# Kernel tuning notes

Hardware: AMD Instinct MI355X
Metric: run time of the kernel (lower is better)

The kernel has to match this reference:

```python
import jax, jax.numpy as jnp
import numpy as np
import math

D = 512          # belief_dim
H = 128          # hidden_dim
R = 64           # relation_dim
M = 8192         # max_beliefs
N = 131072       # candidate pairs
INIT_BIAS = math.log(0.4 / 0.6) * -1.0  # = log(1.5) ~ 0.405465


def _linear_params(key, fan_in, fan_out):
    kw, kb = jax.random.split(key)
    bound = 1.0 / math.sqrt(fan_in)
    W = jax.random.uniform(kw, (fan_in, fan_out), minval=-bound, maxval=bound, dtype=jnp.float32)
    b = jax.random.uniform(kb, (fan_out,), minval=-bound, maxval=bound, dtype=jnp.float32)
    return W, b


def setup_inputs() -> dict:
    key = jax.random.key(0)
    ks = jax.random.split(key, 11)
    beliefs = jax.random.normal(ks[0], (M, D), dtype=jnp.float32)
    src_idx = jax.random.randint(ks[1], (N,), 0, M)
    tgt_idx = jax.random.randint(ks[2], (N,), 0, M)
    # proposal_net: 3D -> H -> H//2 -> 1  (last bias = log(1.5))
    pw1, pb1 = _linear_params(ks[3], 3 * D, H)
    pw2, pb2 = _linear_params(ks[4], H, H // 2)
    pw3, _ = _linear_params(ks[5], H // 2, 1)
    pb3 = jnp.full((1,), INIT_BIAS, dtype=jnp.float32)
    # direction_net: 3D -> H//2 -> 1 (sigmoid)
    dw1, db1 = _linear_params(ks[6], 3 * D, H // 2)
    dw2, db2 = _linear_params(ks[7], H // 2, 1)
    # relation_net: 3D -> H -> R
    rw1, rb1 = _linear_params(ks[8], 3 * D, H)
    rw2, rb2 = _linear_params(ks[9], H, R)
    return {
        "beliefs": beliefs, "src_idx": src_idx, "tgt_idx": tgt_idx,
        "pw1": pw1, "pb1": pb1, "pw2": pw2, "pb2": pb2, "pw3": pw3, "pb3": pb3,
        "dw1": dw1, "db1": db1, "dw2": dw2, "db2": db2,
        "rw1": rw1, "rb1": rb1, "rw2": rw2, "rb2": rb2,
    }


def reference(beliefs, src_idx, tgt_idx,
              pw1, pb1, pw2, pb2, pw3, pb3,
              dw1, db1, dw2, db2,
              rw1, rb1, rw2, rb2):
    src = beliefs[src_idx]                       # [N, D] gather
    tgt = beliefs[tgt_idx]                       # [N, D] gather
    feats = jnp.concatenate([src, tgt, jnp.abs(src - tgt)], axis=-1)  # [N, 3D]

    # proposal head -> edge probability
    h = jax.nn.relu(feats @ pw1 + pb1)
    h = jax.nn.relu(h @ pw2 + pb2)
    probs = jax.nn.sigmoid((h @ pw3 + pb3)[:, 0])                     # [N]

    # direction head -> angle in [0, pi/2]
    d = jax.nn.relu(feats @ dw1 + db1)
    directions = jax.nn.sigmoid((d @ dw2 + db2)[:, 0]) * (jnp.pi / 2)  # [N]

    # relation head -> initial relation vectors
    r = jax.nn.relu(feats @ rw1 + rb1)
    relations = r @ rw2 + rb2                                          # [N, R]

    return probs, directions, relations
```

## Files before the change

kernel.cpp:

```cpp
#include <hip/hip_runtime.h>
#include <hip/hip_bf16.h>


#define DD 512
#define K3 1536
#define ROWS 128
#define RB3 64
#define LDACT 328
#define BUFS 12288
#define BUFS2 16384
#define BUFS3 8192

typedef short bf16x8 __attribute__((ext_vector_type(8)));
typedef float f32x4 __attribute__((ext_vector_type(4)));

__device__ inline float b2f(short s) {
    union { float f; unsigned u; } v;
    v.u = ((unsigned)(unsigned short)s) << 16;
    return v.f;
}
__device__ inline short f2b(float f) {
    union { float fl; unsigned u; } v;
    v.fl = f;
    unsigned x = v.u;
    unsigned r = x + 0x7fffu + ((x >> 16) & 1u);
    return (short)(r >> 16);
}
__device__ inline short babsdiff(short a, short b) {
    union { float f; unsigned u; } v;
    v.f = b2f(a) - b2f(b);
    return (short)((v.u & 0x7fffffffu) >> 16);
}
__device__ __forceinline__ bf16x8 babs8(bf16x8 s, bf16x8 t) {
    bf16x8 a;
#pragma unroll
    for (int j = 0; j < 8; j++) a[j] = babsdiff(s[j], t[j]);
    return a;
}

__device__ __forceinline__ int sidx32(int seg, int rt, int lane) {
    return ((seg * 8 + rt) * 64 + lane) * 8;
}
__device__ __forceinline__ void writeStage(short* buf, int rtw, int lnw, int kcb,
                                           bf16x8 s0, bf16x8 s1,
                                           bf16x8 t0, bf16x8 t1) {
    bf16x8 a0 = babs8(s0, t0), a1 = babs8(s1, t1);
    int l0 = kcb * 16 + lnw, l1 = l0 + 16;
    *(bf16x8*)&buf[sidx32(0, rtw, l0)] = s0;
    *(bf16x8*)&buf[sidx32(0, rtw, l1)] = s1;
    *(bf16x8*)&buf[sidx32(1, rtw, l0)] = t0;
    *(bf16x8*)&buf[sidx32(1, rtw, l1)] = t1;
    *(bf16x8*)&buf[sidx32(2, rtw, l0)] = a0;
    *(bf16x8*)&buf[sidx32(2, rtw, l1)] = a1;
}
__device__ __forceinline__ void stage_f32(const float* bs, const float* bt,
                                          short* buf, int rtw, int lnw, int kcb) {
#pragma unroll
    for (int c = 0; c < 2; c++) {
        bf16x8 sb, tb, ab;
#pragma unroll
        for (int h = 0; h < 2; h++) {
            float4 s4 = ((const float4*)bs)[c * 2 + h];
            float4 t4 = ((const float4*)bt)[c * 2 + h];
            float ss[4] = {s4.x, s4.y, s4.z, s4.w};
            float tt[4] = {t4.x, t4.y, t4.z, t4.w};
#pragma unroll
            for (int e = 0; e < 4; e++) {
                int j = h * 4 + e;
                sb[j] = f2b(ss[e]);
                tb[j] = f2b(tt[e]);
                ab[j] = f2b(fabsf(ss[e] - tt[e]));
            }
        }
        int l16 = (kcb + c) * 16 + lnw;
        *(bf16x8*)&buf[sidx32(0, rtw, l16)] = sb;
        *(bf16x8*)&buf[sidx32(1, rtw, l16)] = tb;
        *(bf16x8*)&buf[sidx32(2, rtw, l16)] = ab;
    }
}

#define WT_ELEMS (320 * 1536)
#define P2T_OFF WT_ELEMS
#define R2T_OFF (WT_ELEMS + 64 * 128)
#define PREP_TOT (WT_ELEMS + 2 * 64 * 128)
#define BEL_ELEMS (8192 * 512)
#define BEL_OFF PREP_TOT

__global__ void prep_kernel(const float* __restrict__ pw1,
                            const float* __restrict__ dw1,
                            const float* __restrict__ rw1,
                            const float* __restrict__ pw2,
                            const float* __restrict__ rw2,
                            const float* __restrict__ beliefs,
                            short* __restrict__ ws, int total8) {
    int i8 = blockIdx.x * 256 + threadIdx.x;
    if (i8 >= total8) return;
    int i = i8 * 8;
    bf16x8 o;
    if (i < WT_ELEMS) {
        int n = i / K3, k = i - n * K3;
        const float* src;
        int stride, off;
        if (n < 128)      { src = pw1; stride = 128; off = n; }
        else if (n < 192) { src = dw1; stride = 64;  off = n - 128; }
        else              { src = rw1; stride = 128; off = n - 192; }
#pragma unroll
        for (int j = 0; j < 8; j++) o[j] = f2b(src[(k + j) * stride + off]);
    } else if (i < R2T_OFF) {
        int jj = i - P2T_OFF;
        int n = jj >> 7, k = jj & 127;
#pragma unroll
        for (int j = 0; j < 8; j++) o[j] = f2b(pw2[(k + j) * 64 + n]);
    } else if (i < PREP_TOT) {
        int jj = i - R2T_OFF;
        int n = jj >> 7, k = jj & 127;
#pragma unroll
        for (int j = 0; j < 8; j++) o[j] = f2b(rw2[(k + j) * 64 + n]);
    } else {
        const float4* b4 = (const float4*)(beliefs + (i - BEL_OFF));
        float4 x = b4[0], y = b4[1];
        float v[8] = {x.x, x.y, x.z, x.w, y.x, y.y, y.z, y.w};
#pragma unroll
        for (int j = 0; j < 8; j++) o[j] = f2b(v[j]);
    }
    *(bf16x8*)&ws[i] = o;
}

__global__ __launch_bounds__(256) void prep_bst(
    const short* __restrict__ bel16, const short* __restrict__ WT,
    float* __restrict__ Bs, float* __restrict__ Bt) {
    const int tb = blockIdx.x & 1;
    const int r0 = (blockIdx.x >> 1) * 32;
    const int t = threadIdx.x;
    const int w = t >> 6, lane = t & 63, q = lane >> 4, ln = lane & 15;
    float* Bo = tb ? Bt : Bs;
    const int koff = tb ? 512 : 0;

    f32x4 acc[5][2];
#pragma unroll
    for (int ct = 0; ct < 5; ct++)
#pragma unroll
        for (int rt = 0; rt < 2; rt++) acc[ct][rt] = (f32x4)(0.f);

#pragma unroll
    for (int k0 = 0; k0 < 512; k0 += 128)
#pragma unroll
        for (int kk = 0; kk < 4; kk++) {
            bf16x8 bfr[5];
#pragma unroll
            for (int ct = 0; ct < 5; ct++)
                bfr[ct] = *(const bf16x8*)(WT + (size_t)(w * 80 + ct * 16 + ln) * K3 +
                                           koff + k0 + kk * 32 + q * 8);
#pragma unroll
            for (int rt = 0; rt < 2; rt++) {
                bf16x8 af = *(const bf16x8*)(bel16 +
                    (size_t)(r0 + rt * 16 + ln) * DD + k0 + kk * 32 + q * 8);
#pragma unroll
                for (int ct = 0; ct < 5; ct++)
                    acc[ct][rt] = __builtin_amdgcn_mfma_f32_16x16x32_bf16(
                        af, bfr[ct], acc[ct][rt], 0, 0, 0);
            }
        }
#pragma unroll
    for (int ct = 0; ct < 5; ct++)
#pragma unroll
        for (int rt = 0; rt < 2; rt++)
#pragma unroll
            for (int i = 0; i < 4; i++)
                Bo[(size_t)(r0 + rt * 16 + q * 4 + i) * 320 +
                   w * 80 + ct * 16 + ln] = acc[ct][rt][i];
}

__global__ __launch_bounds__(256, 3) void edge_main3(
    const short* __restrict__ bel16,
    const int* __restrict__ src_idx, const int* __restrict__ tgt_idx,
    const float* __restrict__ Bs, const float* __restrict__ Bt,
    const float* __restrict__ pb1, const float* __restrict__ db1,
    const float* __restrict__ rb1,
    const float* __restrict__ pb2, const float* __restrict__ pw3,
    const float* __restrict__ pb3,
    const float* __restrict__ dw2, const float* __restrict__ db2,
    const float* __restrict__ rb2,
    const short* __restrict__ WT, const short* __restrict__ pw2T,
    const short* __restrict__ rw2T,
    float* __restrict__ out, int N)
{
    __shared__ __align__(16) char smem_u[32768];
    __shared__ int sIdxR[RB3], tIdxR[RB3];
    short* As = (short*)smem_u;
    short (*acts)[LDACT] = (short (*)[LDACT])smem_u;

    const int t = threadIdx.x;
    const int r0 = blockIdx.x * RB3;
    const int w = t >> 6, lane = t & 63, q = lane >> 4, ln = lane & 15;

    if (t < RB3) sIdxR[t] = src_idx[r0 + t];
    else if (t < 2 * RB3) tIdxR[t - RB3] = tgt_idx[r0 + t - RB3];
    __syncthreads();

    const int rr = t >> 2, cc = t & 3;
    const int rtw = rr >> 4, lnw = rr & 15;
    const size_t srow = (size_t)sIdxR[rr] * DD;
    const size_t trow = (size_t)tIdxR[rr] * DD;

    f32x4 acc[5][4];
#pragma unroll
    for (int ct = 0; ct < 5; ct++)
#pragma unroll
        for (int rt = 0; rt < 4; rt++) acc[ct][rt] = (f32x4)(0.f);

#pragma unroll
    for (int qd = 0; qd < 4; qd++) {
        bf16x8 s8 = *(const bf16x8*)(bel16 + srow + cc * 32 + qd * 8);
        bf16x8 t8 = *(const bf16x8*)(bel16 + trow + cc * 32 + qd * 8);
        bf16x8 a8 = babs8(s8, t8);
        *(bf16x8*)&As[((cc * 4 + rtw) * 64 + qd * 16 + lnw) * 8] = a8;
    }
    __syncthreads();

#pragma unroll
    for (int step = 0; step < 4; step++) {
        short* bufC = As + (step & 1) * BUFS3;
        short* bufN = As + ((step & 1) ^ 1) * BUFS3;
        const int k0 = step * 128;
        const bool pf = (step < 3);
        bf16x8 ps, pt;

#pragma unroll
        for (int kk = 0; kk < 4; kk++) {
            bf16x8 bfr[5];
#pragma unroll
            for (int ct = 0; ct < 5; ct++)
                bfr[ct] = *(const bf16x8*)(WT + (size_t)(w * 80 + ct * 16 + ln) * K3 +
                                           1024 + k0 + kk * 32 + q * 8);
            __builtin_amdgcn_sched_barrier(0);
            if (pf) {
                if (kk > 0) {
                    bf16x8 a8 = babs8(ps, pt);
                    *(bf16x8*)&bufN[((cc * 4 + rtw) * 64 + (kk - 1) * 16 + lnw) * 8] = a8;
                }
                ps = *(const bf16x8*)(bel16 + srow + k0 + 128 + cc * 32 + kk * 8);
                pt = *(const bf16x8*)(bel16 + trow + k0 + 128 + cc * 32 + kk * 8);
            }
            __builtin_amdgcn_sched_barrier(0);
            __builtin_amdgcn_s_setprio(1);
#pragma unroll
            for (int rt = 0; rt < 4; rt++) {
                bf16x8 af = *(const bf16x8*)&bufC[((kk * 4 + rt) * 64 + lane) * 8];
#pragma unroll
                for (int ct = 0; ct < 5; ct++)
                    acc[ct][rt] = __builtin_amdgcn_mfma_f32_16x16x32_bf16(
                        af, bfr[ct], acc[ct][rt], 0, 0, 0);
            }
            __builtin_amdgcn_s_setprio(0);
        }
        if (pf) {
            bf16x8 a8 = babs8(ps, pt);
            *(bf16x8*)&bufN[((cc * 4 + rtw) * 64 + 3 * 16 + lnw) * 8] = a8;
        }
        __syncthreads();
    }

#pragma unroll
    for (int hh = 0; hh < 2; hh++) {
        float bias5[5];
#pragma unroll
        for (int ct = 0; ct < 5; ct++) {
            int col = w * 80 + ct * 16 + ln;
            bias5[ct] = (col < 128) ? pb1[col]
                      : (col < 192) ? db1[col - 128]
                                    : rb1[col - 192];
        }
#pragma unroll
        for (int rt2 = 0; rt2 < 2; rt2++)
#pragma unroll
            for (int i = 0; i < 4; i++) {
                int lrow = rt2 * 16 + q * 4 + i;
                const float* bsp = Bs + (size_t)sIdxR[hh * 32 + lrow] * 320 +
                                   w * 80 + ln;
                const float* btp = Bt + (size_t)tIdxR[hh * 32 + lrow] * 320 +
                                   w * 80 + ln;
#pragma unroll
                for (int ct = 0; ct < 5; ct++) {
                    float v = acc[ct][hh * 2 + rt2][i] +
                              bsp[ct * 16] + btp[ct * 16] + bias5[ct];
                    acts[lrow][w * 80 + ct * 16 + ln] = f2b(fmaxf(v, 0.f));
                }
            }
        __syncthreads();

        {
            f32x4 rc[2];
#pragma unroll
            for (int rt2 = 0; rt2 < 2; rt2++) rc[rt2] = (f32x4)(0.f);
#pragma unroll
            for (int ks = 0; ks < 4; ks++) {
                bf16x8 bfr = *(const bf16x8*)(rw2T + (w * 16 + ln) * 128 +
                                              ks * 32 + q * 8);
#pragma unroll
                for (int rt2 = 0; rt2 < 2; rt2++) {
                    bf16x8 afr = *(const bf16x8*)&acts[rt2 * 16 + ln][192 + ks * 32 + q * 8];
                    rc[rt2] = __builtin_amdgcn_mfma_f32_16x16x32_bf16(afr, bfr, rc[rt2], 0, 0, 0);
                }
            }
            int col = w * 16 + ln;
            float bias = rb2[col];
            float* rel = out + 2 * (size_t)N;
#pragma unroll
            for (int rt2 = 0; rt2 < 2; rt2++)
#pragma unroll
                for (int i = 0; i < 4; i++) {
                    int grow = r0 + hh * 32 + rt2 * 16 + q * 4 + i;
                    rel[(size_t)grow * 64 + col] = rc[rt2][i] + bias;
                }
        }

        f32x4 pc[2];
        {
#pragma unroll
            for (int rt2 = 0; rt2 < 2; rt2++) pc[rt2] = (f32x4)(0.f);
#pragma unroll
            for (int ks = 0; ks < 4; ks++) {
                bf16x8 bfr = *(const bf16x8*)(pw2T + (w * 16 + ln) * 128 +
                                              ks * 32 + q * 8);
#pragma unroll
                for (int rt2 = 0; rt2 < 2; rt2++) {
                    bf16x8 afr = *(const bf16x8*)&acts[rt2 * 16 + ln][0 + ks * 32 + q * 8];
                    pc[rt2] = __builtin_amdgcn_mfma_f32_16x16x32_bf16(afr, bfr, pc[rt2], 0, 0, 0);
                }
            }
        }
        __syncthreads();

        {
            int col = w * 16 + ln;
            float bias = pb2[col];
#pragma unroll
            for (int rt2 = 0; rt2 < 2; rt2++)
#pragma unroll
                for (int i = 0; i < 4; i++) {
                    int lrow = rt2 * 16 + q * 4 + i;
                    acts[lrow][col] = f2b(fmaxf(pc[rt2][i] + bias, 0.f));
                }
        }
        __syncthreads();

        {
            int role = t >> 7;
            int rloc = (t & 127) >> 2;
            int kq = t & 3;
            float s = 0.f;
            if (role == 0) {
#pragma unroll
                for (int j = 0; j < 16; j++)
                    s += b2f(acts[rloc][kq * 16 + j]) * pw3[kq * 16 + j];
            } else {
#pragma unroll
                for (int j = 0; j < 16; j++)
                    s += b2f(acts[rloc][128 + kq * 16 + j]) * dw2[kq * 16 + j];
            }
            s += __shfl_xor(s, 1);
            s += __shfl_xor(s, 2);
            if (kq == 0) {
                if (role == 0) {
                    float pr = 1.f / (1.f + __expf(-(s + pb3[0])));
                    out[r0 + hh * 32 + rloc] = pr;
                } else {
                    float dir = (1.f / (1.f + __expf(-(s + db2[0])))) *
                                1.57079632679489662f;
                    out[(size_t)N + r0 + hh * 32 + rloc] = dir;
                }
            }
        }
        __syncthreads();
    }
}

template<bool BF>
__global__ __launch_bounds__(256, 2) void edge_main(
    const float* __restrict__ beliefs, const short* __restrict__ bel16,
    const int* __restrict__ src_idx, const int* __restrict__ tgt_idx,
    const float* __restrict__ pb1, const float* __restrict__ db1,
    const float* __restrict__ rb1,
    const float* __restrict__ pb2, const float* __restrict__ pw3,
    const float* __restrict__ pb3,
    const float* __restrict__ dw2, const float* __restrict__ db2,
    const float* __restrict__ rb2,
    const short* __restrict__ WT, const short* __restrict__ pw2T,
    const short* __restrict__ rw2T,
    float* __restrict__ out, int N)
{
    __shared__ __align__(16) char smem_u[49152];
    short* As2 = (short*)smem_u;
    short (*acts)[LDACT] = (short (*)[LDACT])smem_u;
    int* sIdx = (int*)smem_u;
    int* tIdx = sIdx + ROWS;

    const int t = threadIdx.x;
    const int r0 = blockIdx.x * ROWS;
    const int w = t >> 6, lane = t & 63, q = lane >> 4, ln = lane & 15;

    if (t < ROWS) sIdx[t] = src_idx[r0 + t] * DD;
    else tIdx[t - ROWS] = tgt_idx[r0 + t - ROWS] * DD;
    __syncthreads();

    const int rrow = t >> 1, kh = t & 1;
    const int rtw = rrow >> 4, lnw = rrow & 15;
    const int kcb = kh * 2;
    const int srow = sIdx[rrow], trow = tIdx[rrow];
    __syncthreads();

    f32x4 acc[5][8];
#pragma unroll
    for (int ct = 0; ct < 5; ct++)
#pragma unroll
        for (int rt = 0; rt < 8; rt++) acc[ct][rt] = (f32x4)(0.f);

    bf16x8 bfr0[5];
#pragma unroll
    for (int ct = 0; ct < 5; ct++) {
        int col = w * 80 + ct * 16 + ln;
        bfr0[ct] = *(const bf16x8*)(WT + (size_t)col * K3 + q * 8);
    }
    if constexpr (BF) {
        const bf16x8* pS = (const bf16x8*)(bel16 + srow + kh * 16);
        const bf16x8* pT = (const bf16x8*)(bel16 + trow + kh * 16);
        writeStage(As2, rtw, lnw, kcb, pS[0], pS[1], pT[0], pT[1]);
    } else {
        stage_f32(beliefs + srow + kh * 16, beliefs + trow + kh * 16,
                  As2, rtw, lnw, kcb);
    }
    __syncthreads();

    for (int step = 0; step < 16; ++step) {
        short* bufC = As2 + (step & 1) * BUFS;
        short* bufN = As2 + ((step & 1) ^ 1) * BUFS;
        const int k0 = step * 32;
        const bool pf = (step < 15);
        bf16x8 ns0, ns1, nt0, nt1;

#pragma unroll
        for (int seg = 0; seg < 3; seg++) {
            bf16x8 bfr[5];
            if (seg == 0) {
#pragma unroll
                for (int ct = 0; ct < 5; ct++) bfr[ct] = bfr0[ct];
            } else {
#pragma unroll
                for (int ct = 0; ct < 5; ct++) {
                    int col = w * 80 + ct * 16 + ln;
                    bfr[ct] = *(const bf16x8*)(WT + (size_t)col * K3 +
                                               seg * DD + k0 + q * 8);
                }
            }
            if (seg == 2) {
                __builtin_amdgcn_sched_barrier(0);
                if (pf) {
                    if constexpr (BF) {
                        const bf16x8* pS = (const bf16x8*)(bel16 + srow + k0 + 32 + kh * 16);
                        const bf16x8* pT = (const bf16x8*)(bel16 + trow + k0 + 32 + kh * 16);
                        ns0 = pS[0]; ns1 = pS[1]; nt0 = pT[0]; nt1 = pT[1];
                    }
#pragma unroll
                    for (int ct = 0; ct < 5; ct++) {
                        int col = w * 80 + ct * 16 + ln;
                        bfr0[ct] = *(const bf16x8*)(WT + (size_t)col * K3 +
                                                    k0 + 32 + q * 8);
                    }
                }
                __builtin_amdgcn_sched_barrier(0);
            }
            __builtin_amdgcn_s_setprio(1);
#pragma unroll
            for (int rt = 0; rt < 8; rt++) {
                bf16x8 af = *(const bf16x8*)&bufC[sidx32(seg, rt, lane)];
#pragma unroll
                for (int ct = 0; ct < 5; ct++)
                    acc[ct][rt] = __builtin_amdgcn_mfma_f32_16x16x32_bf16(
                        af, bfr[ct], acc[ct][rt], 0, 0, 0);
            }
            __builtin_amdgcn_s_setprio(0);
        }
        if constexpr (BF) {
            if (pf) writeStage(bufN, rtw, lnw, kcb, ns0, ns1, nt0, nt1);
        } else {
            if (pf) stage_f32(beliefs + srow + k0 + 32 + kh * 16,
                              beliefs + trow + k0 + 32 + kh * 16,
                              bufN, rtw, lnw, kcb);
        }
        __syncthreads();
    }

#pragma unroll
    for (int h = 0; h < 2; h++) {
#pragma unroll
        for (int ct = 0; ct < 5; ct++) {
            int col = w * 80 + ct * 16 + ln;
            float bias = (col < 128) ? pb1[col]
                       : (col < 192) ? db1[col - 128]
                                     : rb1[col - 192];
#pragma unroll
            for (int rt4 = 0; rt4 < 4; rt4++)
#pragma unroll
                for (int i = 0; i < 4; i++) {
                    int lrow = rt4 * 16 + q * 4 + i;
                    float v = acc[ct][h * 4 + rt4][i] + bias;
                    acts[lrow][col] = f2b(fmaxf(v, 0.f));
                }
        }
        __syncthreads();
        {
            f32x4 rc[4];
#pragma unroll
            for (int rt = 0; rt < 4; rt++) rc[rt] = (f32x4)(0.f);
#pragma unroll
            for (int ks = 0; ks < 4; ks++) {
                bf16x8 bfr = *(const bf16x8*)(rw2T + (w * 16 + ln) * 128 +
                                              ks * 32 + q * 8);
#pragma unroll
                for (int rt = 0; rt < 4; rt++) {
                    bf16x8 afr = *(const bf16x8*)&acts[rt * 16 + ln][192 + ks * 32 + q * 8];
                    rc[rt] = __builtin_amdgcn_mfma_f32_16x16x32_bf16(afr, bfr, rc[rt], 0, 0, 0);
                }
            }
            int col = w * 16 + ln;
            float bias = rb2[col];
            float* rel = out + 2 * (size_t)N;
#pragma unroll
            for (int rt = 0; rt < 4; rt++)
#pragma unroll
                for (int i = 0; i < 4; i++) {
                    int grow = r0 + h * 64 + rt * 16 + q * 4 + i;
                    rel[(size_t)grow * 64 + col] = rc[rt][i] + bias;
                }
        }
        f32x4 pc[4];
        {
#pragma unroll
            for (int rt = 0; rt < 4; rt++) pc[rt] = (f32x4)(0.f);
#pragma unroll
            for (int ks = 0; ks < 4; ks++) {
                bf16x8 bfr = *(const bf16x8*)(pw2T + (w * 16 + ln) * 128 +
                                              ks * 32 + q * 8);
#pragma unroll
                for (int rt = 0; rt < 4; rt++) {
                    bf16x8 afr = *(const bf16x8*)&acts[rt * 16 + ln][0 + ks * 32 + q * 8];
                    pc[rt] = __builtin_amdgcn_mfma_f32_16x16x32_bf16(afr, bfr, pc[rt], 0, 0, 0);
                }
            }
        }
        __syncthreads();
        {
            int col = w * 16 + ln;
            float bias = pb2[col];
#pragma unroll
            for (int rt = 0; rt < 4; rt++)
#pragma unroll
                for (int i = 0; i < 4; i++) {
                    int lrow = rt * 16 + q * 4 + i;
                    acts[lrow][col] = f2b(fmaxf(pc[rt][i] + bias, 0.f));
                }
        }
        __syncthreads();
        if (t < 64) {
            float s = pb3[0];
#pragma unroll 8
            for (int k = 0; k < 64; k++) s += b2f(acts[t][k]) * pw3[k];
            float pr = 1.f / (1.f + __expf(-s));
            out[r0 + h * 64 + t] = pr;
        } else if (t < 128) {
            int lrow = t - 64;
            float s = db2[0];
#pragma unroll 8
            for (int k = 0; k < 64; k++) s += b2f(acts[lrow][128 + k]) * dw2[k];
            float dir = (1.f / (1.f + __expf(-s))) * 1.57079632679489662f;
            out[(size_t)N + r0 + h * 64 + lrow] = dir;
        }
        __syncthreads();
    }
}

extern "C" void kernel_launch(void* const* d_in, const int* in_sizes, int n_in,
                              void* d_out, int out_size, void* d_ws, size_t ws_size,
                              hipStream_t stream) {
    const float* beliefs = (const float*)d_in[0];
    const int* src = (const int*)d_in[1];
    const int* tgt = (const int*)d_in[2];
    const float* pw1 = (const float*)d_in[3];
    const float* pb1 = (const float*)d_in[4];
    const float* pw2 = (const float*)d_in[5];
    const float* pb2 = (const float*)d_in[6];
    const float* pw3 = (const float*)d_in[7];
    const float* pb3 = (const float*)d_in[8];
    const float* dw1 = (const float*)d_in[9];
    const float* db1 = (const float*)d_in[10];
    const float* dw2 = (const float*)d_in[11];
    const float* db2 = (const float*)d_in[12];
    const float* rw1 = (const float*)d_in[13];
    const float* rb1 = (const float*)d_in[14];
    const float* rw2 = (const float*)d_in[15];
    const float* rb2 = (const float*)d_in[16];

    short* ws = (short*)d_ws;
    short* WT    = ws;
    short* pw2T  = ws + P2T_OFF;
    short* rw2T  = ws + R2T_OFF;
    short* bel16 = ws + BEL_OFF;
    const int N = in_sizes[1];

    const size_t BF_BYTES = (size_t)(PREP_TOT + BEL_ELEMS) * sizeof(short);
    const size_t FULL_BYTES = BF_BYTES + (size_t)2 * 8192 * 320 * sizeof(float);
    const bool useV2 = ws_size >= FULL_BYTES;
    const bool useBf = ws_size >= BF_BYTES;
    const int prepElems = useBf ? (PREP_TOT + BEL_ELEMS) : PREP_TOT;
    const int prep8 = prepElems / 8;

    prep_kernel<<<(prep8 + 255) / 256, 256, 0, stream>>>(
        pw1, dw1, rw1, pw2, rw2, beliefs, ws, prep8);

    if (useV2) {
        float* Bsp = (float*)(ws + PREP_TOT + BEL_ELEMS);
        float* Btp = Bsp + (size_t)8192 * 320;
        prep_bst<<<512, 256, 0, stream>>>(bel16, WT, Bsp, Btp);
        edge_main3<<<N / RB3, 256, 0, stream>>>(
            bel16, src, tgt, Bsp, Btp,
            pb1, db1, rb1, pb2, pw3, pb3, dw2, db2, rb2,
            WT, pw2T, rw2T, (float*)d_out, N);
    } else if (useBf) {
        edge_main<true><<<N / ROWS, 256, 0, stream>>>(
            beliefs, bel16, src, tgt, pb1, db1, rb1, pb2, pw3, pb3,
            dw2, db2, rb2, WT, pw2T, rw2T, (float*)d_out, N);
    } else {
        edge_main<false><<<N / ROWS, 256, 0, stream>>>(
            beliefs, bel16, src, tgt, pb1, db1, rb1, pb2, pw3, pb3,
            dw2, db2, rb2, WT, pw2T, rw2T, (float*)d_out, N);
    }
}
```

Before: 271.3 us.

## Split edge kernel into per-wave 32-row tiles with bf16 precomputed src/tgt tables

The precomputed per-belief src/tgt first-layer projections are now stored as bf16 in a layout that lets each lane fetch its five columns with one 16-byte load. The old fp32 tables used strided scalar loads. The main kernel now gives each wave its own 32 rows and all 320 output columns, using a private LDS slot. This removes block-wide __syncthreads and lets each wave run the |src-tgt| GEMM and all heads on its own. The cost is many more accumulator registers (40 f32x4) at occupancy 2, re-reading all weight fragments per wave, and bf16 rounding of the precomputed partial sums.

```diff
diff --git a/kernel.cpp b/kernel.cpp
--- a/kernel.cpp
+++ b/kernel.cpp
@@ -5,11 +5,9 @@
 #define DD 512
 #define K3 1536
 #define ROWS 128
-#define RB3 64
 #define LDACT 328
 #define BUFS 12288
-#define BUFS2 16384
-#define BUFS3 8192
+#define WSLOT 5376
 
 typedef short bf16x8 __attribute__((ext_vector_type(8)));
 typedef float f32x4 __attribute__((ext_vector_type(4)));
@@ -85,6 +83,7 @@
 #define PREP_TOT (WT_ELEMS + 2 * 64 * 128)
 #define BEL_ELEMS (8192 * 512)
 #define BEL_OFF PREP_TOT
+#define TBL_ELEMS (8192 * 4 * 16 * 8)
 
 __global__ void prep_kernel(const float* __restrict__ pw1,
                             const float* __restrict__ dw1,
@@ -126,21 +125,21 @@
     *(bf16x8*)&ws[i] = o;
 }
 
-__global__ __launch_bounds__(256) void prep_bst(
+__global__ __launch_bounds__(256) void prep_bst3(
     const short* __restrict__ bel16, const short* __restrict__ WT,
-    float* __restrict__ Bs, float* __restrict__ Bt) {
+    short* __restrict__ BsT, short* __restrict__ BtT) {
     const int tb = blockIdx.x & 1;
-    const int r0 = (blockIdx.x >> 1) * 32;
+    const int r0 = (blockIdx.x >> 1) * 64;
     const int t = threadIdx.x;
     const int w = t >> 6, lane = t & 63, q = lane >> 4, ln = lane & 15;
-    float* Bo = tb ? Bt : Bs;
+    short* Bo = tb ? BtT : BsT;
     const int koff = tb ? 512 : 0;
 
-    f32x4 acc[5][2];
+    f32x4 acc[5][4];
 #pragma unroll
     for (int ct = 0; ct < 5; ct++)
 #pragma unroll
-        for (int rt = 0; rt < 2; rt++) acc[ct][rt] = (f32x4)(0.f);
+        for (int rt = 0; rt < 4; rt++) acc[ct][rt] = (f32x4)(0.f);
 
 #pragma unroll
     for (int k0 = 0; k0 < 512; k0 += 128)
@@ -152,7 +151,7 @@
                 bfr[ct] = *(const bf16x8*)(WT + (size_t)(w * 80 + ct * 16 + ln) * K3 +
                                            koff + k0 + kk * 32 + q * 8);
 #pragma unroll
-            for (int rt = 0; rt < 2; rt++) {
+            for (int rt = 0; rt < 4; rt++) {
                 bf16x8 af = *(const bf16x8*)(bel16 +
                     (size_t)(r0 + rt * 16 + ln) * DD + k0 + kk * 32 + q * 8);
 #pragma unroll
@@ -162,19 +161,21 @@
             }
         }
 #pragma unroll
-    for (int ct = 0; ct < 5; ct++)
-#pragma unroll
-        for (int rt = 0; rt < 2; rt++)
-#pragma unroll
-            for (int i = 0; i < 4; i++)
-                Bo[(size_t)(r0 + rt * 16 + q * 4 + i) * 320 +
-                   w * 80 + ct * 16 + ln] = acc[ct][rt][i];
-}
-
-__global__ __launch_bounds__(256, 3) void edge_main3(
+    for (int rt = 0; rt < 4; rt++)
+#pragma unroll
+        for (int i = 0; i < 4; i++) {
+            int r = r0 + rt * 16 + q * 4 + i;
+            size_t base = ((size_t)(r * 4 + w) * 16 + ln) * 8;
+#pragma unroll
+            for (int ct = 0; ct < 5; ct++)
+                Bo[base + ct] = f2b(acc[ct][rt][i]);
+        }
+}
+
+__global__ __launch_bounds__(256, 2) void edge_main4(
     const short* __restrict__ bel16,
     const int* __restrict__ src_idx, const int* __restrict__ tgt_idx,
-    const float* __restrict__ Bs, const float* __restrict__ Bt,
+    const short* __restrict__ BsT, const short* __restrict__ BtT,
     const float* __restrict__ pb1, const float* __restrict__ db1,
     const float* __restrict__ rb1,
     const float* __restrict__ pb2, const float* __restrict__ pw3,
@@ -185,194 +186,179 @@
     const short* __restrict__ rw2T,
     float* __restrict__ out, int N)
 {
-    __shared__ __align__(16) char smem_u[32768];
-    __shared__ int sIdxR[RB3], tIdxR[RB3];
-    short* As = (short*)smem_u;
-    short (*acts)[LDACT] = (short (*)[LDACT])smem_u;
-
+    __shared__ __align__(16) short sm[4 * WSLOT];
     const int t = threadIdx.x;
-    const int r0 = blockIdx.x * RB3;
+    const int r0 = blockIdx.x * ROWS;
     const int w = t >> 6, lane = t & 63, q = lane >> 4, ln = lane & 15;
-
-    if (t < RB3) sIdxR[t] = src_idx[r0 + t];
-    else if (t < 2 * RB3) tIdxR[t - RB3] = tgt_idx[r0 + t - RB3];
-    __syncthreads();
-
-    const int rr = t >> 2, cc = t & 3;
-    const int rtw = rr >> 4, lnw = rr & 15;
-    const size_t srow = (size_t)sIdxR[rr] * DD;
-    const size_t trow = (size_t)tIdxR[rr] * DD;
-
-    f32x4 acc[5][4];
-#pragma unroll
-    for (int ct = 0; ct < 5; ct++)
-#pragma unroll
-        for (int rt = 0; rt < 4; rt++) acc[ct][rt] = (f32x4)(0.f);
-
-#pragma unroll
-    for (int qd = 0; qd < 4; qd++) {
-        bf16x8 s8 = *(const bf16x8*)(bel16 + srow + cc * 32 + qd * 8);
-        bf16x8 t8 = *(const bf16x8*)(bel16 + trow + cc * 32 + qd * 8);
-        bf16x8 a8 = babs8(s8, t8);
-        *(bf16x8*)&As[((cc * 4 + rtw) * 64 + qd * 16 + lnw) * 8] = a8;
-    }
-    __syncthreads();
-
-#pragma unroll
-    for (int step = 0; step < 4; step++) {
-        short* bufC = As + (step & 1) * BUFS3;
-        short* bufN = As + ((step & 1) ^ 1) * BUFS3;
-        const int k0 = step * 128;
-        const bool pf = (step < 3);
-        bf16x8 ps, pt;
-
-#pragma unroll
-        for (int kk = 0; kk < 4; kk++) {
-            bf16x8 bfr[5];
-#pragma unroll
-            for (int ct = 0; ct < 5; ct++)
-                bfr[ct] = *(const bf16x8*)(WT + (size_t)(w * 80 + ct * 16 + ln) * K3 +
-                                           1024 + k0 + kk * 32 + q * 8);
-            __builtin_amdgcn_sched_barrier(0);
-            if (pf) {
-                if (kk > 0) {
-                    bf16x8 a8 = babs8(ps, pt);
-                    *(bf16x8*)&bufN[((cc * 4 + rtw) * 64 + (kk - 1) * 16 + lnw) * 8] = a8;
-                }
-                ps = *(const bf16x8*)(bel16 + srow + k0 + 128 + cc * 32 + kk * 8);
-                pt = *(const bf16x8*)(bel16 + trow + k0 + 128 + cc * 32 + kk * 8);
-            }
-            __builtin_amdgcn_sched_barrier(0);
-            __builtin_amdgcn_s_setprio(1);
-#pragma unroll
-            for (int rt = 0; rt < 4; rt++) {
-                bf16x8 af = *(const bf16x8*)&bufC[((kk * 4 + rt) * 64 + lane) * 8];
-#pragma unroll
-                for (int ct = 0; ct < 5; ct++)
-                    acc[ct][rt] = __builtin_amdgcn_mfma_f32_16x16x32_bf16(
-                        af, bfr[ct], acc[ct][rt], 0, 0, 0);
-            }
-            __builtin_amdgcn_s_setprio(0);
-        }
-        if (pf) {
-            bf16x8 a8 = babs8(ps, pt);
-            *(bf16x8*)&bufN[((cc * 4 + rtw) * 64 + 3 * 16 + lnw) * 8] = a8;
-        }
-        __syncthreads();
-    }
-
+    short* slot = sm + w * WSLOT;
+
+    const int lr = lane >> 1, kh = lane & 1;
+    const int myrow = r0 + w * 32 + lr;
+    const size_t srow = (size_t)src_idx[myrow] * DD + kh * 16;
+    const size_t trow = (size_t)tgt_idx[myrow] * DD + kh * 16;
+    const int rtb = lr >> 4, lnw = lr & 15;
+    const int d0 = (rtb * 64 + (kh * 2) * 16 + lnw) * 8;
+    const int d1 = (rtb * 64 + (kh * 2 + 1) * 16 + lnw) * 8;
+
+    f32x4 acc[20][2];
+#pragma unroll
+    for (int ct = 0; ct < 20; ct++) {
+        acc[ct][0] = (f32x4)(0.f);
+        acc[ct][1] = (f32x4)(0.f);
+    }
+
+    bf16x8 ps0 = *(const bf16x8*)(bel16 + srow);
+    bf16x8 ps1 = *(const bf16x8*)(bel16 + srow + 8);
+    bf16x8 pt0 = *(const bf16x8*)(bel16 + trow);
+    bf16x8 pt1 = *(const bf16x8*)(bel16 + trow + 8);
+    *(bf16x8*)&slot[d0] = babs8(ps0, pt0);
+    *(bf16x8*)&slot[d1] = babs8(ps1, pt1);
+    ps0 = *(const bf16x8*)(bel16 + srow + 32);
+    ps1 = *(const bf16x8*)(bel16 + srow + 40);
+    pt0 = *(const bf16x8*)(bel16 + trow + 32);
+    pt1 = *(const bf16x8*)(bel16 + trow + 40);
+
+    for (int kk = 0; kk < 16; ++kk) {
+        const short* tc = slot + (kk & 1) * 1024;
+        short* tn = slot + ((kk & 1) ^ 1) * 1024;
+        bf16x8 bfr[20];
+#pragma unroll
+        for (int ct = 0; ct < 20; ct++)
+            bfr[ct] = *(const bf16x8*)(WT + (size_t)(ct * 16 + ln) * K3 +
+                                       1024 + kk * 32 + q * 8);
+        __builtin_amdgcn_sched_barrier(0);
+        bf16x8 ns0, ns1, nt0, nt1;
+        if (kk < 14) {
+            ns0 = *(const bf16x8*)(bel16 + srow + (kk + 2) * 32);
+            ns1 = *(const bf16x8*)(bel16 + srow + (kk + 2) * 32 + 8);
+            nt0 = *(const bf16x8*)(bel16 + trow + (kk + 2) * 32);
+            nt1 = *(const bf16x8*)(bel16 + trow + (kk + 2) * 32 + 8);
+        }
+        __builtin_amdgcn_sched_barrier(0);
+        bf16x8 af0 = *(const bf16x8*)&tc[(0 * 64 + lane) * 8];
+        bf16x8 af1 = *(const bf16x8*)&tc[(1 * 64 + lane) * 8];
+        __builtin_amdgcn_s_setprio(1);
+#pragma unroll
+        for (int ct = 0; ct < 20; ct++) {
+            acc[ct][0] = __builtin_amdgcn_mfma_f32_16x16x32_bf16(
+                af0, bfr[ct], acc[ct][0], 0, 0, 0);
+            acc[ct][1] = __builtin_amdgcn_mfma_f32_16x16x32_bf16(
+                af1, bfr[ct], acc[ct][1], 0, 0, 0);
+        }
+        __builtin_amdgcn_s_setprio(0);
+        if (kk < 15) {
+            *(bf16x8*)&tn[d0] = babs8(ps0, pt0);
+            *(bf16x8*)&tn[d1] = babs8(ps1, pt1);
+            ps0 = ns0; ps1 = ns1; pt0 = nt0; pt1 = nt1;
+        }
+    }
+
+    short (*acts)[LDACT] = (short (*)[LDACT])slot;
 #pragma unroll
     for (int hh = 0; hh < 2; hh++) {
-        float bias5[5];
-#pragma unroll
-        for (int ct = 0; ct < 5; ct++) {
-            int col = w * 80 + ct * 16 + ln;
-            bias5[ct] = (col < 128) ? pb1[col]
-                      : (col < 192) ? db1[col - 128]
-                                    : rb1[col - 192];
-        }
-#pragma unroll
-        for (int rt2 = 0; rt2 < 2; rt2++)
-#pragma unroll
-            for (int i = 0; i < 4; i++) {
-                int lrow = rt2 * 16 + q * 4 + i;
-                const float* bsp = Bs + (size_t)sIdxR[hh * 32 + lrow] * 320 +
-                                   w * 80 + ln;
-                const float* btp = Bt + (size_t)tIdxR[hh * 32 + lrow] * 320 +
-                                   w * 80 + ln;
-#pragma unroll
-                for (int ct = 0; ct < 5; ct++) {
-                    float v = acc[ct][hh * 2 + rt2][i] +
-                              bsp[ct * 16] + btp[ct * 16] + bias5[ct];
-                    acts[lrow][w * 80 + ct * 16 + ln] = f2b(fmaxf(v, 0.f));
-                }
-            }
-        __syncthreads();
+#pragma unroll
+        for (int i = 0; i < 4; i++) {
+            int gr = r0 + w * 32 + hh * 16 + q * 4 + i;
+            int si = src_idx[gr], ti = tgt_idx[gr];
+#pragma unroll
+            for (int cg = 0; cg < 4; cg++) {
+                bf16x8 bs8 = *(const bf16x8*)(BsT +
+                    ((size_t)(si * 4 + cg) * 16 + ln) * 8);
+                bf16x8 bt8 = *(const bf16x8*)(BtT +
+                    ((size_t)(ti * 4 + cg) * 16 + ln) * 8);
+#pragma unroll
+                for (int c5 = 0; c5 < 5; c5++) {
+                    int ct = cg * 5 + c5;
+                    int col = ct * 16 + ln;
+                    float bias = (col < 128) ? pb1[col]
+                               : (col < 192) ? db1[col - 128]
+                                             : rb1[col - 192];
+                    float v = acc[ct][hh][i] + b2f(bs8[c5]) + b2f(bt8[c5]) + bias;
+                    acts[q * 4 + i][col] = f2b(fmaxf(v, 0.f));
+                }
+            }
+        }
 
         {
-            f32x4 rc[2];
-#pragma unroll
-            for (int rt2 = 0; rt2 < 2; rt2++) rc[rt2] = (f32x4)(0.f);
+            f32x4 rc[4];
+#pragma unroll
+            for (int c2 = 0; c2 < 4; c2++) rc[c2] = (f32x4)(0.f);
 #pragma unroll
             for (int ks = 0; ks < 4; ks++) {
-                bf16x8 bfr = *(const bf16x8*)(rw2T + (w * 16 + ln) * 128 +
-                                              ks * 32 + q * 8);
-#pragma unroll
-                for (int rt2 = 0; rt2 < 2; rt2++) {
-                    bf16x8 afr = *(const bf16x8*)&acts[rt2 * 16 + ln][192 + ks * 32 + q * 8];
-                    rc[rt2] = __builtin_amdgcn_mfma_f32_16x16x32_bf16(afr, bfr, rc[rt2], 0, 0, 0);
-                }
-            }
-            int col = w * 16 + ln;
-            float bias = rb2[col];
+                bf16x8 afr = *(const bf16x8*)&acts[ln][192 + ks * 32 + q * 8];
+#pragma unroll
+                for (int c2 = 0; c2 < 4; c2++) {
+                    bf16x8 bfr2 = *(const bf16x8*)(rw2T + (c2 * 16 + ln) * 128 +
+                                                   ks * 32 + q * 8);
+                    rc[c2] = __builtin_amdgcn_mfma_f32_16x16x32_bf16(
+                        afr, bfr2, rc[c2], 0, 0, 0);
+                }
+            }
             float* rel = out + 2 * (size_t)N;
 #pragma unroll
-            for (int rt2 = 0; rt2 < 2; rt2++)
+            for (int c2 = 0; c2 < 4; c2++) {
+                int col = c2 * 16 + ln;
+                float bias = rb2[col];
 #pragma unroll
                 for (int i = 0; i < 4; i++) {
-                    int grow = r0 + hh * 32 + rt2 * 16 + q * 4 + i;
-                    rel[(size_t)grow * 64 + col] = rc[rt2][i] + bias;
-                }
-        }
-
-        f32x4 pc[2];
+                    int grow = r0 + w * 32 + hh * 16 + q * 4 + i;
+                    rel[(size_t)grow * 64 + col] = rc[c2][i] + bias;
+                }
+            }
+        }
+
+        f32x4 pc[4];
         {
 #pragma unroll
-            for (int rt2 = 0; rt2 < 2; rt2++) pc[rt2] = (f32x4)(0.f);
+            for (int c2 = 0; c2 < 4; c2++) pc[c2] = (f32x4)(0.f);
 #pragma unroll
             for (int ks = 0; ks < 4; ks++) {
-                bf16x8 bfr = *(const bf16x8*)(pw2T + (w * 16 + ln) * 128 +
-                                              ks * 32 + q * 8);
-#pragma unroll
-                for (int rt2 = 0; rt2 < 2; rt2++) {
-                    bf16x8 afr = *(const bf16x8*)&acts[rt2 * 16 + ln][0 + ks * 32 + q * 8];
-                    pc[rt2] = __builtin_amdgcn_mfma_f32_16x16x32_bf16(afr, bfr, pc[rt2], 0, 0, 0);
-                }
-            }
-        }
-        __syncthreads();
+                bf16x8 afr = *(const bf16x8*)&acts[ln][0 + ks * 32 + q * 8];
+#pragma unroll
+                for (int c2 = 0; c2 < 4; c2++) {
+                    bf16x8 bfr2 = *(const bf16x8*)(pw2T + (c2 * 16 + ln) * 128 +
+                                                   ks * 32 + q * 8);
+                    pc[c2] = __builtin_amdgcn_mfma_f32_16x16x32_bf16(
+                        afr, bfr2, pc[c2], 0, 0, 0);
+                }
+            }
+        }
+#pragma unroll
+        for (int c2 = 0; c2 < 4; c2++) {
+            int col = c2 * 16 + ln;
+            float bias = pb2[col];
+#pragma unroll
+            for (int i = 0; i < 4; i++)
+                acts[q * 4 + i][col] = f2b(fmaxf(pc[c2][i] + bias, 0.f));
+        }
 
         {
-            int col = w * 16 + ln;
-            float bias = pb2[col];
-#pragma unroll
-            for (int rt2 = 0; rt2 < 2; rt2++)
-#pragma unroll
-                for (int i = 0; i < 4; i++) {
-                    int lrow = rt2 * 16 + q * 4 + i;
-                    acts[lrow][col] = f2b(fmaxf(pc[rt2][i] + bias, 0.f));
-                }
-        }
-        __syncthreads();
-
-        {
-            int role = t >> 7;
-            int rloc = (t & 127) >> 2;
-            int kq = t & 3;
+            int role = lane >> 5;
+            int rl = (lane & 31) >> 1;
+            int kq = lane & 1;
             float s = 0.f;
             if (role == 0) {
 #pragma unroll
-                for (int j = 0; j < 16; j++)
-                    s += b2f(acts[rloc][kq * 16 + j]) * pw3[kq * 16 + j];
+                for (int j = 0; j < 32; j++)
+                    s += b2f(acts[rl][kq * 32 + j]) * pw3[kq * 32 + j];
             } else {
 #pragma unroll
-                for (int j = 0; j < 16; j++)
-                    s += b2f(acts[rloc][128 + kq * 16 + j]) * dw2[kq * 16 + j];
+                for (int j = 0; j < 32; j++)
+                    s += b2f(acts[rl][128 + kq * 32 + j]) * dw2[kq * 32 + j];
             }
             s += __shfl_xor(s, 1);
-            s += __shfl_xor(s, 2);
             if (kq == 0) {
+                int grow = r0 + w * 32 + hh * 16 + rl;
                 if (role == 0) {
                     float pr = 1.f / (1.f + __expf(-(s + pb3[0])));
-                    out[r0 + hh * 32 + rloc] = pr;
+                    out[grow] = pr;
                 } else {
                     float dir = (1.f / (1.f + __expf(-(s + db2[0])))) *
                                 1.57079632679489662f;
-                    out[(size_t)N + r0 + hh * 32 + rloc] = dir;
-                }
-            }
-        }
-        __syncthreads();
+                    out[(size_t)N + grow] = dir;
+                }
+            }
+        }
     }
 }
 
@@ -609,30 +595,33 @@
     const int N = in_sizes[1];
 
     const size_t BF_BYTES = (size_t)(PREP_TOT + BEL_ELEMS) * sizeof(short);
-    const size_t FULL_BYTES = BF_BYTES + (size_t)2 * 8192 * 320 * sizeof(float);
-    const bool useV2 = ws_size >= FULL_BYTES;
+    const size_t V2_BYTES = BF_BYTES + (size_t)2 * TBL_ELEMS * sizeof(short);
+    const bool useV2 = ws_size >= V2_BYTES;
     const bool useBf = ws_size >= BF_BYTES;
-    const int prepElems = useBf ? (PREP_TOT + BEL_ELEMS) : PREP_TOT;
-    const int prep8 = prepElems / 8;
-
-    prep_kernel<<<(prep8 + 255) / 256, 256, 0, stream>>>(
-        pw1, dw1, rw1, pw2, rw2, beliefs, ws, prep8);
 
     if (useV2) {
-        float* Bsp = (float*)(ws + PREP_TOT + BEL_ELEMS);
-        float* Btp = Bsp + (size_t)8192 * 320;
-        prep_bst<<<512, 256, 0, stream>>>(bel16, WT, Bsp, Btp);
-        edge_main3<<<N / RB3, 256, 0, stream>>>(
-            bel16, src, tgt, Bsp, Btp,
+        const int prep8 = (PREP_TOT + BEL_ELEMS) / 8;
+        prep_kernel<<<(prep8 + 255) / 256, 256, 0, stream>>>(
+            pw1, dw1, rw1, pw2, rw2, beliefs, ws, prep8);
+        short* BsT = ws + PREP_TOT + BEL_ELEMS;
+        short* BtT = BsT + TBL_ELEMS;
+        prep_bst3<<<256, 256, 0, stream>>>(bel16, WT, BsT, BtT);
+        edge_main4<<<N / ROWS, 256, 0, stream>>>(
+            bel16, src, tgt, BsT, BtT,
             pb1, db1, rb1, pb2, pw3, pb3, dw2, db2, rb2,
             WT, pw2T, rw2T, (float*)d_out, N);
-    } else if (useBf) {
-        edge_main<true><<<N / ROWS, 256, 0, stream>>>(
-            beliefs, bel16, src, tgt, pb1, db1, rb1, pb2, pw3, pb3,
-            dw2, db2, rb2, WT, pw2T, rw2T, (float*)d_out, N);
     } else {
-        edge_main<false><<<N / ROWS, 256, 0, stream>>>(
-            beliefs, bel16, src, tgt, pb1, db1, rb1, pb2, pw3, pb3,
-            dw2, db2, rb2, WT, pw2T, rw2T, (float*)d_out, N);
-    }
-}
+        const int prepElems = useBf ? (PREP_TOT + BEL_ELEMS) : PREP_TOT;
+        const int prep8 = prepElems / 8;
+        prep_kernel<<<(prep8 + 255) / 256, 256, 0, stream>>>(
+            pw1, dw1, rw1, pw2, rw2, beliefs, ws, prep8);
+        if (useBf)
+            edge_main<true><<<N / ROWS, 256, 0, stream>>>(
+                beliefs, bel16, src, tgt, pb1, db1, rb1, pb2, pw3, pb3,
+                dw2, db2, rb2, WT, pw2T, rw2T, (float*)d_out, N);
+        else
+            edge_main<false><<<N / ROWS, 256, 0, stream>>>(
+                beliefs, bel16, src, tgt, pb1, db1, rb1, pb2, pw3, pb3,
+                dw2, db2, rb2, WT, pw2T, rw2T, (float*)d_out, N);
+    }
+}
```

Measured after the change: 579.0 us. +113.4%, slower.
